# Kernel optimization log

Hardware: AMD Instinct MI355X
Metric: run time of the kernel (lower is better)

## Reference

```python
import jax, jax.numpy as jnp
import numpy as np

DELTA_V = 0.1
DELTA_D = 0.5
NUM_LABELS = 33  # label 0 = background, instance ids 1..32


def setup_inputs() -> dict:
    key = jax.random.key(0)
    k1, k2 = jax.random.split(key)
    B, N, D = 8, 131072, 32
    embeddings = jax.random.normal(k1, (B, N, D), dtype=jnp.float32)
    labels = jax.random.randint(k2, (B, N), 0, NUM_LABELS, dtype=jnp.int32)
    return {"embeddings": embeddings, "labels": labels}


def reference(embeddings, labels):
    # embeddings: [B, N, D], labels: [B, N] int (0 = ignore)
    B = embeddings.shape[0]
    dt = embeddings.dtype

    oh = jax.nn.one_hot(labels, NUM_LABELS, dtype=dt)              # [B, N, L]
    counts = oh.sum(1)                                              # [B, L]
    sums = jnp.einsum('bnl,bnd->bld', oh, embeddings)               # [B, L, D]
    means = sums / jnp.maximum(counts, 1.0)[..., None]              # [B, L, D]

    # ---- pull loss: hinge on distance of each point to its instance mean ----
    mean_pt = jnp.take_along_axis(means, labels[..., None], axis=1)  # [B, N, D]
    diff = embeddings - mean_pt
    dist = jnp.sqrt(jnp.sum(diff * diff, -1) + 1e-24)               # [B, N]
    hinge = jnp.maximum(dist - DELTA_V, 0.0)
    seg_mean = jnp.einsum('bnl,bn->bl', oh, hinge) / jnp.maximum(counts, 1.0)  # [B, L]

    present = counts[:, 1:] > 0                                     # [B, L-1]
    n_inst = present.sum(-1).astype(dt)                             # [B]
    pull_b = seg_mean[:, 1:].sum(-1) / (n_inst + 1e-6)
    pull = pull_b.sum() / B

    # ---- push loss: hinge margin between normalized instance means ----
    m = means[:, 1:, :]                                             # [B, L-1, D]
    mn = m / jnp.maximum(jnp.linalg.norm(m, axis=-1, keepdims=True), 1e-12)
    sq = jnp.sum((mn[:, :, None, :] - mn[:, None, :, :]) ** 2, -1)  # [B, K, K]
    dmat = jnp.sqrt(sq + 1e-24)
    K = NUM_LABELS - 1
    triu = jnp.triu(jnp.ones((K, K), dt), 1)
    pmask = triu[None] * present[:, :, None].astype(dt) * present[:, None, :].astype(dt)
    hp = jnp.maximum(2.0 * DELTA_D - dmat, 0.0) * pmask
    push_b = jnp.where(n_inst > 1, hp.sum((-2, -1)) / (pmask.sum((-2, -1)) + 1e-6), 0.0)
    push = push_b.sum() / B

    total = pull + push
    return jnp.stack([total, pull, push])
```

## Files before the change

kernel.cpp:

```cpp
#include <hip/hip_runtime.h>
#include <hip/hip_bf16.h>

#define BATCH 8
#define NPTS  131072
#define DIM   32
#define NLAB  33
#define G1X   128
#define P1PTS 1024
#define BPB2  128

#define OFF_CNT   0
#define OFF_SUM   264
#define OFF_PULL  (264 + 8448)
#define OFF_PSUM  (OFF_PULL + BATCH * BPB2)
#define OFF_PCNT  (OFF_PSUM + BATCH * G1X * NLAB * DIM)
#define WS_FLOATS (OFF_PCNT + BATCH * G1X * NLAB)

typedef short  bf16x8 __attribute__((ext_vector_type(8)));
typedef float  f32x4  __attribute__((ext_vector_type(4)));
typedef int    i32x4  __attribute__((ext_vector_type(4)));

static __device__ __forceinline__ short f2bf(float f) {
  __hip_bfloat16 h = __float2bfloat16(f);
  return *reinterpret_cast<short*>(&h);
}

#define P1_ISSUE(EV, L0, L1, T)                                               \
  {                                                                           \
    const int vt = ve0 + (T) * 4096;                                          \
    const int vl = vl0 + (T) * 128;                                           \
    asm volatile("global_load_dword %0, %1, %2"            : "=&v"(EV[0])  : "v"(vt), "s"(ebase)); \
    asm volatile("global_load_dword %0, %1, %2 offset:128" : "=&v"(EV[1])  : "v"(vt), "s"(ebase)); \
    asm volatile("global_load_dword %0, %1, %2 offset:256" : "=&v"(EV[2])  : "v"(vt), "s"(ebase)); \
    asm volatile("global_load_dword %0, %1, %2 offset:384" : "=&v"(EV[3])  : "v"(vt), "s"(ebase)); \
    asm volatile("global_load_dword %0, %1, %2 offset:512" : "=&v"(EV[4])  : "v"(vt), "s"(ebase)); \
    asm volatile("global_load_dword %0, %1, %2 offset:640" : "=&v"(EV[5])  : "v"(vt), "s"(ebase)); \
    asm volatile("global_load_dword %0, %1, %2 offset:768" : "=&v"(EV[6])  : "v"(vt), "s"(ebase)); \
    asm volatile("global_load_dword %0, %1, %2 offset:896" : "=&v"(EV[7])  : "v"(vt), "s"(ebase)); \
    asm volatile("global_load_dword %0, %1, %2 offset:64"  : "=&v"(EV[8])  : "v"(vt), "s"(ebase)); \
    asm volatile("global_load_dword %0, %1, %2 offset:192" : "=&v"(EV[9])  : "v"(vt), "s"(ebase)); \
    asm volatile("global_load_dword %0, %1, %2 offset:320" : "=&v"(EV[10]) : "v"(vt), "s"(ebase)); \
    asm volatile("global_load_dword %0, %1, %2 offset:448" : "=&v"(EV[11]) : "v"(vt), "s"(ebase)); \
    asm volatile("global_load_dword %0, %1, %2 offset:576" : "=&v"(EV[12]) : "v"(vt), "s"(ebase)); \
    asm volatile("global_load_dword %0, %1, %2 offset:704" : "=&v"(EV[13]) : "v"(vt), "s"(ebase)); \
    asm volatile("global_load_dword %0, %1, %2 offset:832" : "=&v"(EV[14]) : "v"(vt), "s"(ebase)); \
    asm volatile("global_load_dword %0, %1, %2 offset:960" : "=&v"(EV[15]) : "v"(vt), "s"(ebase)); \
    asm volatile("global_load_dwordx4 %0, %1, %2"           : "=&v"(L0) : "v"(vl), "s"(lbase));    \
    asm volatile("global_load_dwordx4 %0, %1, %2 offset:16" : "=&v"(L1) : "v"(vl), "s"(lbase));    \
  }

#define P1_COMPUTE(EV, L0, L1)                                                \
  {                                                                           \
    bf16x8 a0, a1, a2, b0, b1;                                                \
    _Pragma("unroll")                                                         \
    for (int j = 0; j < 8; ++j) {                                             \
      const int lj = (j < 4) ? L0[j] : L1[j - 4];                             \
      const int h0 = (lj == m0), h1 = (lj == m0 + 16), h2 = (lj == m0 + 32);  \
      a0[j] = h0 ? (short)0x3F80 : (short)0;                                  \
      a1[j] = h1 ? (short)0x3F80 : (short)0;                                  \
      a2[j] = h2 ? (short)0x3F80 : (short)0;                                  \
      cnt0 += h0; cnt1 += h1; cnt2 += h2;                                     \
      b0[j] = f2bf(EV[j]);                                                    \
      b1[j] = f2bf(EV[8 + j]);                                                \
    }                                                                         \
    acc[0][0] = __builtin_amdgcn_mfma_f32_16x16x32_bf16(a0, b0, acc[0][0], 0, 0, 0); \
    acc[0][1] = __builtin_amdgcn_mfma_f32_16x16x32_bf16(a0, b1, acc[0][1], 0, 0, 0); \
    acc[1][0] = __builtin_amdgcn_mfma_f32_16x16x32_bf16(a1, b0, acc[1][0], 0, 0, 0); \
    acc[1][1] = __builtin_amdgcn_mfma_f32_16x16x32_bf16(a1, b1, acc[1][1], 0, 0, 0); \
    acc[2][0] = __builtin_amdgcn_mfma_f32_16x16x32_bf16(a2, b0, acc[2][0], 0, 0, 0); \
    acc[2][1] = __builtin_amdgcn_mfma_f32_16x16x32_bf16(a2, b1, acc[2][1], 0, 0, 0); \
  }

#define P1_WAIT(N)                                                            \
  asm volatile("s_waitcnt vmcnt(" #N ")" ::: "memory");                       \
  __builtin_amdgcn_sched_barrier(0);

__global__ __launch_bounds__(256) void pass1_kernel(
    const float* __restrict__ emb, const int* __restrict__ lab,
    float* __restrict__ psum, float* __restrict__ pcnt) {
  const int b    = blockIdx.y;
  const int tid  = threadIdx.x;
  const int w    = __builtin_amdgcn_readfirstlane(tid >> 6);
  const int lane = tid & 63;
  const int m0   = lane & 15;
  const int g    = lane >> 4;

  __shared__ float s_stage[4][NLAB * DIM];
  __shared__ int   s_cnt4[4][NLAB];

  const size_t base = (size_t)b * NPTS + (size_t)blockIdx.x * P1PTS
                    + (size_t)w * 256;
  const float* ebase = emb + base * DIM;
  const int*   lbase = lab + base;
  const int ve0 = g * 1024 + m0 * 4;
  const int vl0 = g * 32;

  f32x4 acc[3][2];
#pragma unroll
  for (int t = 0; t < 3; ++t)
#pragma unroll
    for (int u = 0; u < 2; ++u) acc[t][u] = (f32x4){0.f, 0.f, 0.f, 0.f};
  int cnt0 = 0, cnt1 = 0, cnt2 = 0;

  float eA[16], eB[16], eC[16];
  i32x4 lA0, lA1, lB0, lB1, lC0, lC1;

  P1_ISSUE(eA, lA0, lA1, 0);
  P1_ISSUE(eB, lB0, lB1, 1);
  P1_ISSUE(eC, lC0, lC1, 2);
  P1_WAIT(36); P1_COMPUTE(eA, lA0, lA1); P1_ISSUE(eA, lA0, lA1, 3);
  P1_WAIT(36); P1_COMPUTE(eB, lB0, lB1); P1_ISSUE(eB, lB0, lB1, 4);
  P1_WAIT(36); P1_COMPUTE(eC, lC0, lC1); P1_ISSUE(eC, lC0, lC1, 5);
  P1_WAIT(36); P1_COMPUTE(eA, lA0, lA1); P1_ISSUE(eA, lA0, lA1, 6);
  P1_WAIT(36); P1_COMPUTE(eB, lB0, lB1); P1_ISSUE(eB, lB0, lB1, 7);
  P1_WAIT(36); P1_COMPUTE(eC, lC0, lC1);
  P1_WAIT(18); P1_COMPUTE(eA, lA0, lA1);
  P1_WAIT(0);  P1_COMPUTE(eB, lB0, lB1);

  cnt0 += __shfl_xor(cnt0, 16); cnt0 += __shfl_xor(cnt0, 32);
  cnt1 += __shfl_xor(cnt1, 16); cnt1 += __shfl_xor(cnt1, 32);
  cnt2 += __shfl_xor(cnt2, 16); cnt2 += __shfl_xor(cnt2, 32);
  if (lane < 16)            s_cnt4[w][m0]      = cnt0;
  else if (lane < 32)       s_cnt4[w][m0 + 16] = cnt1;
  if (lane == 32)           s_cnt4[w][32]      = cnt2;

  float* st = s_stage[w];
#pragma unroll
  for (int t = 0; t < 2; ++t)
#pragma unroll
    for (int u = 0; u < 2; ++u)
#pragma unroll
      for (int r = 0; r < 4; ++r)
        st[(t * 16 + g * 4 + r) * DIM + m0 + 16 * u] = acc[t][u][r];
  if (lane < 16) {
    st[32 * DIM + m0]      = acc[2][0][0];
    st[32 * DIM + m0 + 16] = acc[2][1][0];
  }
  __syncthreads();

  const size_t pb = (size_t)b * G1X + blockIdx.x;
  for (int i = tid; i < NLAB * DIM; i += 256) {
    const float v = s_stage[0][i] + s_stage[1][i] + s_stage[2][i] + s_stage[3][i];
    psum[pb * (NLAB * DIM) + i] = v;
  }
  if (tid < NLAB) {
    const int c = s_cnt4[0][tid] + s_cnt4[1][tid] + s_cnt4[2][tid] + s_cnt4[3][tid];
    pcnt[pb * NLAB + tid] = (float)c;
  }
}

__global__ __launch_bounds__(256) void reduce_kernel(
    const float* __restrict__ psum, const float* __restrict__ pcnt,
    float* __restrict__ gsum, float* __restrict__ gcnt) {
  constexpr int TOT = BATCH * NLAB * DIM;
  constexpr int KS  = G1X / 8;
  const int slice = blockIdx.y;
  const int o = blockIdx.x * 256 + threadIdx.x;
  if (o < TOT) {
    const int b = o / (NLAB * DIM), i = o - b * (NLAB * DIM);
    const float* src = psum + ((size_t)b * G1X + slice * KS) * (NLAB * DIM) + i;
    float a0 = 0.f, a1 = 0.f, a2 = 0.f, a3 = 0.f;
#pragma unroll
    for (int k = 0; k < KS; k += 4) {
      a0 += src[(size_t)(k + 0) * (NLAB * DIM)];
      a1 += src[(size_t)(k + 1) * (NLAB * DIM)];
      a2 += src[(size_t)(k + 2) * (NLAB * DIM)];
      a3 += src[(size_t)(k + 3) * (NLAB * DIM)];
    }
    atomicAdd(&gsum[o], (a0 + a1) + (a2 + a3));
  } else if (o - TOT < BATCH * NLAB) {
    const int o2 = o - TOT;
    const int b = o2 / NLAB, l = o2 - b * NLAB;
    const float* src = pcnt + ((size_t)b * G1X + slice * KS) * NLAB + l;
    float a = 0.f;
#pragma unroll
    for (int k = 0; k < KS; ++k) a += src[(size_t)k * NLAB];
    atomicAdd(&gcnt[o2], a);
  }
}

#define CN 8
#define P2_ISSUE(LB, EB, C)                                                   \
  {                                                                           \
    _Pragma("unroll")                                                         \
    for (int j = 0; j < CN; ++j) {                                            \
      const size_t it = (size_t)(C) * CN + j;                                 \
      const unsigned long long al =                                           \
          (unsigned long long)(lab + base + p0 + it * PSTRIDE);               \
      asm volatile("global_load_dword %0, %1, off" : "=&v"(LB[j]) : "v"(al)); \
    }                                                                         \
    _Pragma("unroll")                                                         \
    for (int j = 0; j < CN; ++j) {                                            \
      const size_t it = (size_t)(C) * CN + j;                                 \
      const unsigned long long ae =                                           \
          (unsigned long long)(emb + (base + p0 + it * PSTRIDE) * DIM + d0);  \
      asm volatile("global_load_dwordx4 %0, %1, off" : "=&v"(EB[j]) : "v"(ae)); \
    }                                                                         \
  }

#define P2_COMPUTE(LB, EB)                                                    \
  {                                                                           \
    float s[CN];                                                              \
    _Pragma("unroll")                                                         \
    for (int j = 0; j < CN; ++j) {                                            \
      const f32x4 mv = *(const f32x4*)(s_mean + LB[j] * 36 + d0);             \
      const float dx = EB[j][0] - mv[0], dy = EB[j][1] - mv[1];               \
      const float dz = EB[j][2] - mv[2], dw = EB[j][3] - mv[3];               \
      s[j] = dx * dx + dy * dy + dz * dz + dw * dw;                           \
    }                                                                         \
    _Pragma("unroll")                                                         \
    for (int j = 0; j < CN; ++j) {                                            \
      s[j] += __shfl_xor(s[j], 1);                                            \
      s[j] += __shfl_xor(s[j], 2);                                            \
      s[j] += __shfl_xor(s[j], 4);                                            \
    }                                                                         \
    float sv = s[0];                                                          \
    int   lv = LB[0];                                                         \
    _Pragma("unroll")                                                         \
    for (int j = 1; j < CN; ++j) {                                            \
      sv = (lane8 == j) ? s[j] : sv;                                          \
      lv = (lane8 == j) ? LB[j] : lv;                                         \
    }                                                                         \
    const float dist = sqrtf(sv + 1e-24f);                                    \
    wacc += s_w[lv] * fmaxf(dist - 0.1f, 0.f);                                \
  }

__global__ __launch_bounds__(256, 4) void pass2_kernel(
    const float* __restrict__ emb, const int* __restrict__ lab,
    const float* __restrict__ gsum, const float* __restrict__ gcnt,
    float* __restrict__ pull_part) {
  const int b   = blockIdx.y;
  const int tid = threadIdx.x;
  __shared__ __align__(16) float s_mean[NLAB * 36];
  __shared__ float s_w[NLAB];
  __shared__ float s_red[4];

  for (int i = tid; i < NLAB * DIM; i += 256) {
    const int l = i >> 5, d = i & 31;
    const float c = gcnt[b * NLAB + l];
    s_mean[l * 36 + d] = gsum[b * (NLAB * DIM) + i] / fmaxf(c, 1.0f);
  }
  if (tid < 64) {
    const float c = (tid < NLAB) ? gcnt[b * NLAB + tid] : 0.f;
    const int pres = (tid >= 1 && tid < NLAB && c > 0.f) ? 1 : 0;
    const unsigned long long bal = __ballot(pres);
    const float n_inst = (float)__popcll(bal);
    if (tid < NLAB)
      s_w[tid] = pres ? 1.f / (fmaxf(c, 1.f) * (n_inst + 1e-6f)) : 0.f;
  }
  __syncthreads();

  const int sub   = tid >> 3;
  const int lane8 = tid & 7;
  const int d0    = lane8 << 2;
  const size_t base = (size_t)b * NPTS;
  const int p0 = blockIdx.x * 32 + sub;
  constexpr int PSTRIDE = BPB2 * 32;
  constexpr int NIT     = NPTS / PSTRIDE;
  constexpr int NCH     = NIT / CN;

  int   labsA[CN], labsB[CN];
  f32x4 eA[CN], eB[CN];
  float wacc = 0.f;

  P2_ISSUE(labsA, eA, 0);
#pragma unroll
  for (int cc = 0; cc < NCH; cc += 2) {
    if (cc + 1 < NCH) P2_ISSUE(labsB, eB, cc + 1);
    if (cc + 1 < NCH) { asm volatile("s_waitcnt vmcnt(16)" ::: "memory"); }
    else              { asm volatile("s_waitcnt vmcnt(0)"  ::: "memory"); }
    __builtin_amdgcn_sched_barrier(0);
    P2_COMPUTE(labsA, eA);
    if (cc + 1 < NCH) {
      if (cc + 2 < NCH) P2_ISSUE(labsA, eA, cc + 2);
      if (cc + 2 < NCH) { asm volatile("s_waitcnt vmcnt(16)" ::: "memory"); }
      else              { asm volatile("s_waitcnt vmcnt(0)"  ::: "memory"); }
      __builtin_amdgcn_sched_barrier(0);
      P2_COMPUTE(labsB, eB);
    }
  }

#pragma unroll
  for (int mm = 1; mm < 64; mm <<= 1) wacc += __shfl_xor(wacc, mm);
  if ((tid & 63) == 0) s_red[tid >> 6] = wacc;
  __syncthreads();
  if (tid == 0)
    pull_part[b * BPB2 + blockIdx.x] =
        s_red[0] + s_red[1] + s_red[2] + s_red[3];
}

__global__ __launch_bounds__(512) void finish_kernel(
    const float* __restrict__ gsum, const float* __restrict__ gcnt,
    const float* __restrict__ pull_part, float* __restrict__ out) {
  const int tid = threadIdx.x;
  const int b   = tid >> 6;
  const int t   = tid & 63;
  __shared__ __align__(16) float s_mn[BATCH * 32 * DIM];
  __shared__ float s_ps[BATCH];
  __shared__ float s_pl[BATCH];
  float* mn = s_mn + b * 32 * DIM;

  {
    float plsum = pull_part[b * BPB2 + t] + pull_part[b * BPB2 + 64 + t];
#pragma unroll
    for (int m = 1; m < 64; m <<= 1) plsum += __shfl_xor(plsum, m);
    if (t == 0) s_pl[b] = plsum;
  }

  int pres = 0;
  if (t < 32) {
    const int l = t + 1;
    const float cnt = gcnt[b * NLAB + l];
    pres = (cnt > 0.f) ? 1 : 0;
    const float inv = 1.f / fmaxf(cnt, 1.f);
    float v[DIM];
    float n2 = 0.f;
    for (int d = 0; d < DIM; d++) {
      v[d] = gsum[b * (NLAB * DIM) + l * DIM + d] * inv;
      n2  += v[d] * v[d];
    }
    const float scale = 1.f / fmaxf(sqrtf(n2), 1e-12f);
    for (int d = 0; d < DIM; d++) mn[t * DIM + d] = v[d] * scale;
  }
  const unsigned long long bal = __ballot(pres);
  const unsigned int pmask32 = (unsigned int)(bal & 0xFFFFFFFFull);
  const int n_inst = __popc(pmask32);

  __syncthreads();

  float hp_sum = 0.f, pm_sum = 0.f;
  for (int idx = t; idx < 1024; idx += 64) {
    const int i = idx >> 5, j = idx & 31;
    if (j > i && ((pmask32 >> i) & 1u) && ((pmask32 >> j) & 1u)) {
      const float4* a = (const float4*)(mn + i * DIM);
      const float4* c = (const float4*)(mn + j * DIM);
      float sq = 0.f;
      for (int q = 0; q < 8; q++) {
        const float4 av = a[q], cv = c[q];
        const float dx = av.x - cv.x, dy = av.y - cv.y;
        const float dz = av.z - cv.z, dw = av.w - cv.w;
        sq += dx * dx + dy * dy + dz * dz + dw * dw;
      }
      const float dmat = sqrtf(sq + 1e-24f);
      hp_sum += fmaxf(1.0f - dmat, 0.f);
      pm_sum += 1.f;
    }
  }
  for (int m = 1; m < 64; m <<= 1) {
    hp_sum += __shfl_xor(hp_sum, m);
    pm_sum += __shfl_xor(pm_sum, m);
  }
  const float push = (n_inst > 1) ? hp_sum / (pm_sum + 1e-6f) : 0.f;
  if (t == 0) s_ps[b] = push;
  __syncthreads();

  if (tid < 64) {
    float pl = (t < BATCH) ? s_pl[t] : 0.f;
    float ps = (t < BATCH) ? s_ps[t] : 0.f;
#pragma unroll
    for (int m = 1; m < 64; m <<= 1) {
      pl += __shfl_xor(pl, m);
      ps += __shfl_xor(ps, m);
    }
    if (t == 0) {
      const float pull_m = pl / (float)BATCH;
      const float push_m = ps / (float)BATCH;
      out[0] = pull_m + push_m;
      out[1] = pull_m;
      out[2] = push_m;
    }
  }
}

extern "C" void kernel_launch(void* const* d_in, const int* in_sizes, int n_in,
                              void* d_out, int out_size, void* d_ws, size_t ws_size,
                              hipStream_t stream) {
  const float* emb = (const float*)d_in[0];
  const int*   lab = (const int*)d_in[1];
  float* out = (float*)d_out;
  float* ws  = (float*)d_ws;

  float* gcnt  = ws + OFF_CNT;
  float* gsum  = ws + OFF_SUM;
  float* pullp = ws + OFF_PULL;
  float* psum  = ws + OFF_PSUM;
  float* pcnt  = ws + OFF_PCNT;

  hipMemsetAsync(d_ws, 0, (OFF_SUM + BATCH * NLAB * DIM) * sizeof(float), stream);

  dim3 grid1(G1X, BATCH);
  dim3 gridR((BATCH * NLAB * DIM + BATCH * NLAB + 255) / 256, 8);
  dim3 grid2(BPB2, BATCH);
  pass1_kernel<<<grid1, 256, 0, stream>>>(emb, lab, psum, pcnt);
  reduce_kernel<<<gridR, 256, 0, stream>>>(psum, pcnt, gsum, gcnt);
  pass2_kernel<<<grid2, 256, 0, stream>>>(emb, lab, gsum, gcnt, pullp);
  finish_kernel<<<1, 512, 0, stream>>>(gsum, gcnt, pullp, out);
}
```

Baseline: 232.7 us.

## Load embeddings with dwordx4 and transpose through LDS for MFMA B fragments

Replaces the sixteen strided dword global loads per tile with four coalesced dwordx4 loads. The tile is staged into a padded per-wave LDS buffer and read back transposed to build the bf16 B operands. Pipeline depth drops from three register buffers to two, with LDS double-buffering. This trades fewer, wider memory requests for extra LDS traffic and less load prefetch in flight.

```diff
diff --git a/kernel.cpp b/kernel.cpp
--- a/kernel.cpp
+++ b/kernel.cpp
@@ -18,6 +18,7 @@
 
 typedef short  bf16x8 __attribute__((ext_vector_type(8)));
 typedef float  f32x4  __attribute__((ext_vector_type(4)));
+typedef float  f32x2  __attribute__((ext_vector_type(2)));
 typedef int    i32x4  __attribute__((ext_vector_type(4)));
 
 static __device__ __forceinline__ short f2bf(float f) {
@@ -25,33 +26,35 @@
   return *reinterpret_cast<short*>(&h);
 }
 
+#define P1_WAIT(N)                                                            \
+  asm volatile("s_waitcnt vmcnt(" #N ")" ::: "memory");                       \
+  __builtin_amdgcn_sched_barrier(0);
+
 #define P1_ISSUE(EV, L0, L1, T)                                               \
   {                                                                           \
-    const int vt = ve0 + (T) * 4096;                                          \
-    const int vl = vl0 + (T) * 128;                                           \
-    asm volatile("global_load_dword %0, %1, %2"            : "=&v"(EV[0])  : "v"(vt), "s"(ebase)); \
-    asm volatile("global_load_dword %0, %1, %2 offset:128" : "=&v"(EV[1])  : "v"(vt), "s"(ebase)); \
-    asm volatile("global_load_dword %0, %1, %2 offset:256" : "=&v"(EV[2])  : "v"(vt), "s"(ebase)); \
-    asm volatile("global_load_dword %0, %1, %2 offset:384" : "=&v"(EV[3])  : "v"(vt), "s"(ebase)); \
-    asm volatile("global_load_dword %0, %1, %2 offset:512" : "=&v"(EV[4])  : "v"(vt), "s"(ebase)); \
-    asm volatile("global_load_dword %0, %1, %2 offset:640" : "=&v"(EV[5])  : "v"(vt), "s"(ebase)); \
-    asm volatile("global_load_dword %0, %1, %2 offset:768" : "=&v"(EV[6])  : "v"(vt), "s"(ebase)); \
-    asm volatile("global_load_dword %0, %1, %2 offset:896" : "=&v"(EV[7])  : "v"(vt), "s"(ebase)); \
-    asm volatile("global_load_dword %0, %1, %2 offset:64"  : "=&v"(EV[8])  : "v"(vt), "s"(ebase)); \
-    asm volatile("global_load_dword %0, %1, %2 offset:192" : "=&v"(EV[9])  : "v"(vt), "s"(ebase)); \
-    asm volatile("global_load_dword %0, %1, %2 offset:320" : "=&v"(EV[10]) : "v"(vt), "s"(ebase)); \
-    asm volatile("global_load_dword %0, %1, %2 offset:448" : "=&v"(EV[11]) : "v"(vt), "s"(ebase)); \
-    asm volatile("global_load_dword %0, %1, %2 offset:576" : "=&v"(EV[12]) : "v"(vt), "s"(ebase)); \
-    asm volatile("global_load_dword %0, %1, %2 offset:704" : "=&v"(EV[13]) : "v"(vt), "s"(ebase)); \
-    asm volatile("global_load_dword %0, %1, %2 offset:832" : "=&v"(EV[14]) : "v"(vt), "s"(ebase)); \
-    asm volatile("global_load_dword %0, %1, %2 offset:960" : "=&v"(EV[15]) : "v"(vt), "s"(ebase)); \
-    asm volatile("global_load_dwordx4 %0, %1, %2"           : "=&v"(L0) : "v"(vl), "s"(lbase));    \
-    asm volatile("global_load_dwordx4 %0, %1, %2 offset:16" : "=&v"(L1) : "v"(vl), "s"(lbase));    \
-  }
-
-#define P1_COMPUTE(EV, L0, L1)                                                \
-  {                                                                           \
-    bf16x8 a0, a1, a2, b0, b1;                                                \
+    const int vt  = ve + (T) * 4096;                                          \
+    const int vlt = vl + (T) * 128;                                           \
+    asm volatile("global_load_dwordx4 %0, %1, %2"             : "=&v"(EV[0]) : "v"(vt),  "s"(ebase)); \
+    asm volatile("global_load_dwordx4 %0, %1, %2 offset:1024" : "=&v"(EV[1]) : "v"(vt),  "s"(ebase)); \
+    asm volatile("global_load_dwordx4 %0, %1, %2 offset:2048" : "=&v"(EV[2]) : "v"(vt),  "s"(ebase)); \
+    asm volatile("global_load_dwordx4 %0, %1, %2 offset:3072" : "=&v"(EV[3]) : "v"(vt),  "s"(ebase)); \
+    asm volatile("global_load_dwordx4 %0, %1, %2"             : "=&v"(L0)    : "v"(vlt), "s"(lbase)); \
+    asm volatile("global_load_dwordx4 %0, %1, %2 offset:16"   : "=&v"(L1)    : "v"(vlt), "s"(lbase)); \
+  }
+
+#define P1_STAGE(EV, BUF)                                                     \
+  {                                                                           \
+    float* st_ = s_st[w][BUF];                                                \
+    _Pragma("unroll")                                                         \
+    for (int r = 0; r < 4; ++r) {                                             \
+      const int idx = (r * 8 + (lane >> 3)) * 34 + (lane & 7) * 4;            \
+      *(f32x2*)&st_[idx]     = (f32x2){EV[r][0], EV[r][1]};                   \
+      *(f32x2*)&st_[idx + 2] = (f32x2){EV[r][2], EV[r][3]};                   \
+    }                                                                         \
+  }
+
+#define P1_FRAGA(L0, L1)                                                      \
+  {                                                                           \
     _Pragma("unroll")                                                         \
     for (int j = 0; j < 8; ++j) {                                             \
       const int lj = (j < 4) ? L0[j] : L1[j - 4];                             \
@@ -60,8 +63,17 @@
       a1[j] = h1 ? (short)0x3F80 : (short)0;                                  \
       a2[j] = h2 ? (short)0x3F80 : (short)0;                                  \
       cnt0 += h0; cnt1 += h1; cnt2 += h2;                                     \
-      b0[j] = f2bf(EV[j]);                                                    \
-      b1[j] = f2bf(EV[8 + j]);                                                \
+    }                                                                         \
+  }
+
+#define P1_BMFMA(BUF)                                                         \
+  {                                                                           \
+    const float* st_ = s_st[w][BUF];                                          \
+    bf16x8 b0, b1;                                                            \
+    _Pragma("unroll")                                                         \
+    for (int j = 0; j < 8; ++j) {                                             \
+      b0[j] = f2bf(st_[(g * 8 + j) * 34 + m0]);                               \
+      b1[j] = f2bf(st_[(g * 8 + j) * 34 + m0 + 16]);                          \
     }                                                                         \
     acc[0][0] = __builtin_amdgcn_mfma_f32_16x16x32_bf16(a0, b0, acc[0][0], 0, 0, 0); \
     acc[0][1] = __builtin_amdgcn_mfma_f32_16x16x32_bf16(a0, b1, acc[0][1], 0, 0, 0); \
@@ -70,10 +82,6 @@
     acc[2][0] = __builtin_amdgcn_mfma_f32_16x16x32_bf16(a2, b0, acc[2][0], 0, 0, 0); \
     acc[2][1] = __builtin_amdgcn_mfma_f32_16x16x32_bf16(a2, b1, acc[2][1], 0, 0, 0); \
   }
-
-#define P1_WAIT(N)                                                            \
-  asm volatile("s_waitcnt vmcnt(" #N ")" ::: "memory");                       \
-  __builtin_amdgcn_sched_barrier(0);
 
 __global__ __launch_bounds__(256) void pass1_kernel(
     const float* __restrict__ emb, const int* __restrict__ lab,
@@ -85,15 +93,15 @@
   const int m0   = lane & 15;
   const int g    = lane >> 4;
 
-  __shared__ float s_stage[4][NLAB * DIM];
+  __shared__ float s_st[4][2][1088];
   __shared__ int   s_cnt4[4][NLAB];
 
   const size_t base = (size_t)b * NPTS + (size_t)blockIdx.x * P1PTS
                     + (size_t)w * 256;
   const float* ebase = emb + base * DIM;
   const int*   lbase = lab + base;
-  const int ve0 = g * 1024 + m0 * 4;
-  const int vl0 = g * 32;
+  const int ve = (lane >> 3) * 128 + (lane & 7) * 16;
+  const int vl = g * 32;
 
   f32x4 acc[3][2];
 #pragma unroll
@@ -101,21 +109,22 @@
 #pragma unroll
     for (int u = 0; u < 2; ++u) acc[t][u] = (f32x4){0.f, 0.f, 0.f, 0.f};
   int cnt0 = 0, cnt1 = 0, cnt2 = 0;
-
-  float eA[16], eB[16], eC[16];
-  i32x4 lA0, lA1, lB0, lB1, lC0, lC1;
+  bf16x8 a0, a1, a2;
+
+  f32x4 eA[4], eB[4];
+  i32x4 lA0, lA1, lB0, lB1;
 
   P1_ISSUE(eA, lA0, lA1, 0);
   P1_ISSUE(eB, lB0, lB1, 1);
-  P1_ISSUE(eC, lC0, lC1, 2);
-  P1_WAIT(36); P1_COMPUTE(eA, lA0, lA1); P1_ISSUE(eA, lA0, lA1, 3);
-  P1_WAIT(36); P1_COMPUTE(eB, lB0, lB1); P1_ISSUE(eB, lB0, lB1, 4);
-  P1_WAIT(36); P1_COMPUTE(eC, lC0, lC1); P1_ISSUE(eC, lC0, lC1, 5);
-  P1_WAIT(36); P1_COMPUTE(eA, lA0, lA1); P1_ISSUE(eA, lA0, lA1, 6);
-  P1_WAIT(36); P1_COMPUTE(eB, lB0, lB1); P1_ISSUE(eB, lB0, lB1, 7);
-  P1_WAIT(36); P1_COMPUTE(eC, lC0, lC1);
-  P1_WAIT(18); P1_COMPUTE(eA, lA0, lA1);
-  P1_WAIT(0);  P1_COMPUTE(eB, lB0, lB1);
+
+  P1_WAIT(6); P1_STAGE(eA, 0); P1_FRAGA(lA0, lA1); P1_ISSUE(eA, lA0, lA1, 2); P1_BMFMA(0);
+  P1_WAIT(6); P1_STAGE(eB, 1); P1_FRAGA(lB0, lB1); P1_ISSUE(eB, lB0, lB1, 3); P1_BMFMA(1);
+  P1_WAIT(6); P1_STAGE(eA, 0); P1_FRAGA(lA0, lA1); P1_ISSUE(eA, lA0, lA1, 4); P1_BMFMA(0);
+  P1_WAIT(6); P1_STAGE(eB, 1); P1_FRAGA(lB0, lB1); P1_ISSUE(eB, lB0, lB1, 5); P1_BMFMA(1);
+  P1_WAIT(6); P1_STAGE(eA, 0); P1_FRAGA(lA0, lA1); P1_ISSUE(eA, lA0, lA1, 6); P1_BMFMA(0);
+  P1_WAIT(6); P1_STAGE(eB, 1); P1_FRAGA(lB0, lB1); P1_ISSUE(eB, lB0, lB1, 7); P1_BMFMA(1);
+  P1_WAIT(6); P1_STAGE(eA, 0); P1_FRAGA(lA0, lA1); P1_BMFMA(0);
+  P1_WAIT(0); P1_STAGE(eB, 1); P1_FRAGA(lB0, lB1); P1_BMFMA(1);
 
   cnt0 += __shfl_xor(cnt0, 16); cnt0 += __shfl_xor(cnt0, 32);
   cnt1 += __shfl_xor(cnt1, 16); cnt1 += __shfl_xor(cnt1, 32);
@@ -124,7 +133,7 @@
   else if (lane < 32)       s_cnt4[w][m0 + 16] = cnt1;
   if (lane == 32)           s_cnt4[w][32]      = cnt2;
 
-  float* st = s_stage[w];
+  float* st = &s_st[w][0][0];
 #pragma unroll
   for (int t = 0; t < 2; ++t)
 #pragma unroll
@@ -140,7 +149,7 @@
 
   const size_t pb = (size_t)b * G1X + blockIdx.x;
   for (int i = tid; i < NLAB * DIM; i += 256) {
-    const float v = s_stage[0][i] + s_stage[1][i] + s_stage[2][i] + s_stage[3][i];
+    const float v = s_st[0][0][i] + s_st[1][0][i] + s_st[2][0][i] + s_st[3][0][i];
     psum[pb * (NLAB * DIM) + i] = v;
   }
   if (tid < NLAB) {
```

Measured after the change: 233.8 us. About the same (+0.5%).
